# Kernel optimization log

Measured on AMD Instinct MI355X. Metric: run time of the kernel, lower is better.

The kernel has to match this reference:

```python
import jax, jax.numpy as jnp
import numpy as np

N_NODES = 100000
N_EDGES = 600000
D = 128
L = 4
BN_EPS = 1e-5


def setup_inputs() -> dict:
    key = jax.random.key(0)
    ks = jax.random.split(key, 12)
    x = jax.random.normal(ks[0], (N_NODES, D), dtype=jnp.float32)
    edge_index = jax.random.randint(ks[1], (2, N_EDGES), 0, N_NODES, dtype=jnp.int64)
    edge_attr = jax.random.uniform(ks[2], (N_EDGES, 1), dtype=jnp.float32)
    s = 0.05
    return {
        'x': x,
        'edge_index': edge_index,
        'edge_attr': edge_attr,
        'We': jax.random.normal(ks[3], (L, 1, D), dtype=jnp.float32) * s,   # GINE edge projection Linear(1, D)
        'be': jnp.zeros((L, D), dtype=jnp.float32),
        'eps': jnp.zeros((L,), dtype=jnp.float32),                          # train_eps=True, init 0
        'W1': jax.random.normal(ks[4], (L, D, D), dtype=jnp.float32) * s,
        'b1': jnp.zeros((L, D), dtype=jnp.float32),
        'gamma': jnp.ones((L, D), dtype=jnp.float32),
        'beta': jnp.zeros((L, D), dtype=jnp.float32),
        'W2': jax.random.normal(ks[5], (L, D, D), dtype=jnp.float32) * s,
        'b2': jnp.zeros((L, D), dtype=jnp.float32),
    }


def _gine_layer(h, src, dst, edge_attr, We, be, eps, W1, b1, gamma, beta, W2, b2):
    n = h.shape[0]
    e = edge_attr @ We + be                       # [E, D] edge embedding
    m = jax.nn.relu(h[src] + e)                   # gather + add + relu (messages)
    agg = jax.ops.segment_sum(m, dst, num_segments=n)  # scatter-add to destination nodes
    z = (1.0 + eps) * h + agg
    # MLP: Linear -> BatchNorm1d (training stats) -> ReLU -> Linear
    z = z @ W1 + b1
    mu = jnp.mean(z, axis=0)
    var = jnp.var(z, axis=0)                      # biased var, as in torch BN training
    z = (z - mu) * jax.lax.rsqrt(var + BN_EPS) * gamma + beta
    z = jax.nn.relu(z)
    return z @ W2 + b2


def reference(x, edge_index, edge_attr, We, be, eps, W1, b1, gamma, beta, W2, b2):
    src, dst = edge_index[0], edge_index[1]
    h = x
    for l in range(L):
        z = _gine_layer(h, src, dst, edge_attr, We[l], be[l], eps[l],
                        W1[l], b1[l], gamma[l], beta[l], W2[l], b2[l])
        r = jax.nn.relu(z)
        h = r if l == 0 else h + r
    return h
```

## Files before the change

kernel.cpp:

```cpp
#include <hip/hip_runtime.h>

#define NN 100000
#define NE 600000
#define DD 128
#define NL 4
#define GB 512

typedef __attribute__((ext_vector_type(8))) short short8;
typedef __attribute__((ext_vector_type(4))) float float4v;

__device__ inline unsigned short f2bf(float f) {
  union { float f; unsigned u; } v; v.f = f;
  unsigned r = v.u + 0x7fff + ((v.u >> 16) & 1);
  return (unsigned short)(r >> 16);
}
__device__ inline float bf2f(unsigned short u) {
  union { unsigned u; float f; } v; v.u = ((unsigned)u) << 16;
  return v.f;
}

__global__ void k_h2b(const float* __restrict__ src, unsigned short* __restrict__ dst,
                      float* __restrict__ stats4, int* __restrict__ counts) {
  int i = blockIdx.x * 256 + threadIdx.x;
  if (i < NL * 256) stats4[i] = 0.f;
  if (i < NN) counts[i] = 0;
  if (i >= NN * DD / 4) return;
  float4 v = ((const float4*)src)[i];
  ushort4 o;
  o.x = f2bf(v.x); o.y = f2bf(v.y); o.z = f2bf(v.z); o.w = f2bf(v.w);
  ((ushort4*)dst)[i] = o;
}

__global__ void k_prep(const float* __restrict__ W1, const float* __restrict__ W2,
                       unsigned short* __restrict__ WT) {
  int i = blockIdx.x * 256 + threadIdx.x;
  if (i >= 8 * 16384) return;
  int m = i >> 14;
  int el = i & 16383;
  int k = el >> 7;
  int n = el & 127;
  const float* src = (m < 4) ? (W1 + (size_t)m * 16384) : (W2 + (size_t)(m - 4) * 16384);
  WT[(size_t)m * 16384 + n * 128 + k] = f2bf(src[k * 128 + n]);
}

__global__ void k_count(const int* __restrict__ ei, int* __restrict__ counts) {
  int e = blockIdx.x * 256 + threadIdx.x;
  if (e < NE) atomicAdd(&counts[ei[NE + e]], 1);
}

#define ST 256
#define SC 2
#define SB ((NN + ST * SC - 1) / (ST * SC))

__global__ void k_scan_part(const int* __restrict__ counts, int* __restrict__ row_ptr,
                            int* __restrict__ bsums) {
  __shared__ int s[ST];
  int b = blockIdx.x, t = threadIdx.x;
  int base = b * (ST * SC) + t * SC;
  int v0 = (base < NN) ? counts[base] : 0;
  int v1 = (base + 1 < NN) ? counts[base + 1] : 0;
  int tsum = v0 + v1;
  s[t] = tsum;
  __syncthreads();
  for (int d = 1; d < ST; d <<= 1) {
    int x = (t >= d) ? s[t - d] : 0;
    __syncthreads();
    s[t] += x;
    __syncthreads();
  }
  int excl = s[t] - tsum;
  if (base < NN) row_ptr[base] = excl;
  if (base + 1 < NN) row_ptr[base + 1] = excl + v0;
  if (t == ST - 1) bsums[b] = s[t];
}

__global__ void k_scan_bsum(const int* __restrict__ bsums, int* __restrict__ boffs,
                            int* __restrict__ row_ptr) {
  __shared__ int s[ST];
  int t = threadIdx.x;
  int v = (t < SB) ? bsums[t] : 0;
  s[t] = v;
  __syncthreads();
  for (int d = 1; d < ST; d <<= 1) {
    int x = (t >= d) ? s[t - d] : 0;
    __syncthreads();
    s[t] += x;
    __syncthreads();
  }
  if (t < SB) boffs[t] = s[t] - v;
  if (t == ST - 1) row_ptr[NN] = s[t];
}

__global__ void k_scan_add(const int* __restrict__ boffs, int* __restrict__ row_ptr,
                           int* __restrict__ off) {
  int b = blockIdx.x, t = threadIdx.x;
  int base = b * (ST * SC) + t * SC;
  int o = boffs[b];
  if (base < NN) { row_ptr[base] += o; off[base] = 0; }
  if (base + 1 < NN) { row_ptr[base + 1] += o; off[base + 1] = 0; }
}

__global__ void k_fill(const int* __restrict__ ei, const float* __restrict__ attr,
                       const int* __restrict__ row_ptr, int* __restrict__ off,
                       int2* __restrict__ csr) {
  int e = blockIdx.x * 256 + threadIdx.x;
  if (e >= NE) return;
  int srcv = ei[e];
  int dstv = ei[NE + e];
  int pos = atomicAdd(&off[dstv], 1);
  int idx = row_ptr[dstv] + pos;
  csr[idx] = make_int2(srcv, __float_as_int(attr[e]));
}

__global__ void k_agg(const unsigned short* __restrict__ hb,
                      const int* __restrict__ row_ptr, const int2* __restrict__ csr,
                      const float* __restrict__ We, const float* __restrict__ be,
                      const float* __restrict__ epsp, unsigned short* __restrict__ zb) {
  int gid = blockIdx.x * blockDim.x + threadIdx.x;
  int n = gid >> 6;
  int lane = gid & 63;
  if (n >= NN) return;
  int d0 = lane * 2;
  float we0 = We[d0], we1 = We[d0 + 1];
  float be0 = be[d0], be1 = be[d0 + 1];
  int b = row_ptr[n], e = row_ptr[n + 1];
  int deg = e - b;
  int cnt = (deg < 64) ? deg : 64;
  int2 rec = (lane < cnt) ? csr[b + lane] : make_int2(0, 0);
  int myidx = rec.x;
  float myatt = __int_as_float(rec.y);
  if (lane >= cnt) myatt = 0.f;
  float acc0 = 0.f, acc1 = 0.f;
  int i = 0;
  for (; i + 4 <= cnt; i += 4) {
    int s0 = __shfl(myidx, i);
    int s1 = __shfl(myidx, i + 1);
    int s2 = __shfl(myidx, i + 2);
    int s3 = __shfl(myidx, i + 3);
    float a0 = __shfl(myatt, i);
    float a1 = __shfl(myatt, i + 1);
    float a2 = __shfl(myatt, i + 2);
    float a3 = __shfl(myatt, i + 3);
    unsigned hv0 = *(const unsigned*)(hb + (size_t)s0 * DD + d0);
    unsigned hv1 = *(const unsigned*)(hb + (size_t)s1 * DD + d0);
    unsigned hv2 = *(const unsigned*)(hb + (size_t)s2 * DD + d0);
    unsigned hv3 = *(const unsigned*)(hb + (size_t)s3 * DD + d0);
    acc0 += fmaxf(bf2f((unsigned short)(hv0 & 0xffffu)) + fmaf(a0, we0, be0), 0.f);
    acc1 += fmaxf(bf2f((unsigned short)(hv0 >> 16)) + fmaf(a0, we1, be1), 0.f);
    acc0 += fmaxf(bf2f((unsigned short)(hv1 & 0xffffu)) + fmaf(a1, we0, be0), 0.f);
    acc1 += fmaxf(bf2f((unsigned short)(hv1 >> 16)) + fmaf(a1, we1, be1), 0.f);
    acc0 += fmaxf(bf2f((unsigned short)(hv2 & 0xffffu)) + fmaf(a2, we0, be0), 0.f);
    acc1 += fmaxf(bf2f((unsigned short)(hv2 >> 16)) + fmaf(a2, we1, be1), 0.f);
    acc0 += fmaxf(bf2f((unsigned short)(hv3 & 0xffffu)) + fmaf(a3, we0, be0), 0.f);
    acc1 += fmaxf(bf2f((unsigned short)(hv3 >> 16)) + fmaf(a3, we1, be1), 0.f);
  }
  for (; i < cnt; i++) {
    int s = __shfl(myidx, i);
    float a = __shfl(myatt, i);
    unsigned hv = *(const unsigned*)(hb + (size_t)s * DD + d0);
    acc0 += fmaxf(bf2f((unsigned short)(hv & 0xffffu)) + fmaf(a, we0, be0), 0.f);
    acc1 += fmaxf(bf2f((unsigned short)(hv >> 16)) + fmaf(a, we1, be1), 0.f);
  }
  for (int j = b + 64; j < e; j++) {
    int2 r2 = csr[j];
    float a = __int_as_float(r2.y);
    unsigned hv = *(const unsigned*)(hb + (size_t)r2.x * DD + d0);
    acc0 += fmaxf(bf2f((unsigned short)(hv & 0xffffu)) + fmaf(a, we0, be0), 0.f);
    acc1 += fmaxf(bf2f((unsigned short)(hv >> 16)) + fmaf(a, we1, be1), 0.f);
  }
  float ep = 1.f + epsp[0];
  unsigned hs = *(const unsigned*)(hb + (size_t)n * DD + d0);
  float zx = fmaf(ep, bf2f((unsigned short)(hs & 0xffffu)), acc0);
  float zy = fmaf(ep, bf2f((unsigned short)(hs >> 16)), acc1);
  unsigned pk = (unsigned)f2bf(zx) | ((unsigned)f2bf(zy) << 16);
  *(unsigned*)(zb + (size_t)n * DD + d0) = pk;
}

template <int MODE>
__global__ __launch_bounds__(256, 2) void k_gemm(
    const unsigned short* __restrict__ Xb, const unsigned short* __restrict__ WT,
    const float* __restrict__ bias, float* __restrict__ stats,
    const float* __restrict__ gamma, const float* __restrict__ beta,
    const float* __restrict__ hprev, float* __restrict__ Yout,
    unsigned short* __restrict__ Ybf) {
  __shared__ unsigned short Wl[128 * 136];
  __shared__ unsigned short Xl[2][64 * 136];
  __shared__ float bns[256];
  const int tid = threadIdx.x;
  const int G = gridDim.x;
  const int NT = (NN + 63) >> 6;

  for (int i = tid; i < 2048; i += 256) {
    int rr = i >> 4, c = i & 15;
    *(uint4*)&Wl[rr * 136 + c * 8] = *(const uint4*)&WT[rr * 128 + c * 8];
  }

  const int lane = tid & 63;
  const int w = tid >> 6;
  const int m = lane & 15;
  const int quad = lane >> 4;

  const int c8 = tid & 15, rr16 = tid >> 4;
  float scl[8], sfl[8];
  if (MODE >= 1) {
    if (tid < 128) {
      const float invN = 1.f / (float)NN;
      float mu = stats[tid] * invN;
      float var = fmaxf(stats[128 + tid] * invN - mu * mu, 0.f);
      float xx = var + 1e-5f;
      float r = rsqrtf(xx);
      r = r * (1.5f - 0.5f * xx * r * r);
      float scale = gamma[tid] * r;
      bns[tid] = scale;
      bns[128 + tid] = beta[tid] - mu * scale;
    }
    __syncthreads();
#pragma unroll
    for (int j = 0; j < 8; j++) {
      scl[j] = bns[c8 * 8 + j];
      sfl[j] = bns[128 + c8 * 8 + j];
    }
  }

  uint4 xu[4];
  auto LOADR = [&](int t) {
    int r0 = t << 6;
#pragma unroll
    for (int it = 0; it < 4; it++) {
      int gr = r0 + rr16 + it * 16;
      xu[it] = (gr < NN) ? *(const uint4*)(Xb + (size_t)gr * DD + c8 * 8)
                         : make_uint4(0u, 0u, 0u, 0u);
    }
  };
  auto STORE_LDS = [&](int b) {
#pragma unroll
    for (int it = 0; it < 4; it++) {
      int row = rr16 + it * 16;
      uint4 u = xu[it];
      if (MODE >= 1) {
        unsigned p[4] = {u.x, u.y, u.z, u.w};
#pragma unroll
        for (int j = 0; j < 4; j++) {
          float lo = bf2f((unsigned short)(p[j] & 0xffffu));
          float hi = bf2f((unsigned short)(p[j] >> 16));
          lo = fmaxf(fmaf(lo, scl[2 * j], sfl[2 * j]), 0.f);
          hi = fmaxf(fmaf(hi, scl[2 * j + 1], sfl[2 * j + 1]), 0.f);
          p[j] = (unsigned)f2bf(lo) | ((unsigned)f2bf(hi) << 16);
        }
        u = make_uint4(p[0], p[1], p[2], p[3]);
      }
      *(uint4*)&Xl[b][row * 136 + c8 * 8] = u;
    }
  };

  float4v ssum[8], ssq[8];
  if (MODE == 0) {
#pragma unroll
    for (int ct = 0; ct < 8; ct++) {
      ssum[ct] = (float4v){0.f, 0.f, 0.f, 0.f};
      ssq[ct] = (float4v){0.f, 0.f, 0.f, 0.f};
    }
  }

  const int t0 = blockIdx.x;
  LOADR(t0);
  STORE_LDS(0);
  if (t0 + G < NT) LOADR(t0 + G);
  __syncthreads();

  int buf = 0;
  for (int t = t0; t < NT; t += G) {
    const int nxt = t + G;
    if (nxt < NT) {
      STORE_LDS(buf ^ 1);
      if (nxt + G < NT) LOADR(nxt + G);
    }

    float4v acc[8];
#pragma unroll
    for (int ct = 0; ct < 8; ct++) {
      float4 b4 = *(const float4*)&bias[ct * 16 + quad * 4];
      acc[ct] = (float4v){b4.x, b4.y, b4.z, b4.w};
    }

    const unsigned short* Ap = &Wl[m * 136 + quad * 8];
    const unsigned short* Bp = &Xl[buf][(w * 16 + m) * 136 + quad * 8];
#pragma unroll
    for (int q = 0; q < 4; q++) {
      short8 bfrag = *(const short8*)(Bp + q * 32);
#pragma unroll
      for (int ct = 0; ct < 8; ct++) {
        short8 afrag = *(const short8*)(Ap + ct * 16 * 136 + q * 32);
        acc[ct] = __builtin_amdgcn_mfma_f32_16x16x32_bf16(afrag, bfrag, acc[ct], 0, 0, 0);
      }
    }

    asm volatile("s_waitcnt lgkmcnt(0)" ::: "memory");
    __builtin_amdgcn_s_barrier();

    const int r = (t << 6) + w * 16 + m;
    if (r < NN) {
      const size_t rb = (size_t)r * DD;
#pragma unroll
      for (int ct = 0; ct < 8; ct++) {
        float4v v = acc[ct];
        const int col = ct * 16 + quad * 4;
        if (MODE == 0) {
          ssum[ct] += v;
          ssq[ct] += v * v;
          ushort4 o;
          o.x = f2bf(v[0]); o.y = f2bf(v[1]); o.z = f2bf(v[2]); o.w = f2bf(v[3]);
          *(ushort4*)&Ybf[rb + col] = o;
        } else {
          v[0] = fmaxf(v[0], 0.f); v[1] = fmaxf(v[1], 0.f);
          v[2] = fmaxf(v[2], 0.f); v[3] = fmaxf(v[3], 0.f);
          if (MODE == 2) {
            float4 hp = *(const float4*)&hprev[rb + col];
            v[0] += hp.x; v[1] += hp.y; v[2] += hp.z; v[3] += hp.w;
          }
          *(float4v*)&Yout[rb + col] = v;
          if (Ybf) {
            ushort4 o;
            o.x = f2bf(v[0]); o.y = f2bf(v[1]); o.z = f2bf(v[2]); o.w = f2bf(v[3]);
            *(ushort4*)&Ybf[rb + col] = o;
          }
        }
      }
    }
    buf ^= 1;
  }

  if (MODE == 0) {
    float* sarr = (float*)Xl;
    float* sqarr = sarr + 512;
#pragma unroll
    for (int ct = 0; ct < 8; ct++) {
      float4v s = ssum[ct], s2 = ssq[ct];
#pragma unroll
      for (int d = 1; d < 16; d <<= 1) {
#pragma unroll
        for (int j = 0; j < 4; j++) {
          s[j] += __shfl_xor(s[j], d);
          s2[j] += __shfl_xor(s2[j], d);
        }
      }
      if (m == 0) {
        *(float4v*)&sarr[w * 128 + ct * 16 + quad * 4] = s;
        *(float4v*)&sqarr[w * 128 + ct * 16 + quad * 4] = s2;
      }
    }
    __syncthreads();
    if (tid < 128) {
      atomicAdd(&stats[tid], sarr[tid] + sarr[128 + tid] + sarr[256 + tid] + sarr[384 + tid]);
    } else {
      int c = tid - 128;
      atomicAdd(&stats[128 + c], sqarr[c] + sqarr[128 + c] + sqarr[256 + c] + sqarr[384 + c]);
    }
  }
}

static inline size_t align256(size_t x) { return (x + 255) & ~(size_t)255; }

extern "C" void kernel_launch(void* const* d_in, const int* in_sizes, int n_in,
                              void* d_out, int out_size, void* d_ws, size_t ws_size,
                              hipStream_t stream) {
  const float* x     = (const float*)d_in[0];
  const int*   ei    = (const int*)d_in[1];
  const float* attr  = (const float*)d_in[2];
  const float* We    = (const float*)d_in[3];
  const float* be    = (const float*)d_in[4];
  const float* eps   = (const float*)d_in[5];
  const float* W1    = (const float*)d_in[6];
  const float* b1    = (const float*)d_in[7];
  const float* gamma = (const float*)d_in[8];
  const float* beta  = (const float*)d_in[9];
  const float* W2    = (const float*)d_in[10];
  const float* b2    = (const float*)d_in[11];
  float* out = (float*)d_out;

  char* w = (char*)d_ws;
  unsigned short* z2 = (unsigned short*)w; w += align256((size_t)NN * DD * 2);
  unsigned short* hb = (unsigned short*)w; w += align256((size_t)NN * DD * 2);
  unsigned short* zb = (unsigned short*)w; w += align256((size_t)NN * DD * 2);
  int*   row_ptr  = (int*)w;   w += align256((size_t)(NN + 1) * 4);
  int*   counts   = (int*)w;   w += align256((size_t)NN * 4);
  int*   off      = (int*)w;   w += align256((size_t)NN * 4);
  int2*  csr      = (int2*)w;  w += align256((size_t)NE * 8);
  float* stats4   = (float*)w; w += align256((size_t)NL * 256 * 4);
  int*   bsums    = (int*)w;   w += align256(ST * 4);
  int*   boffs    = (int*)w;   w += align256(ST * 4);
  unsigned short* WTb = (unsigned short*)w; w += align256((size_t)8 * 16384 * 2);

  k_prep<<<512, 256, 0, stream>>>(W1, W2, WTb);
  k_h2b<<<(NN * DD / 4 + 255) / 256, 256, 0, stream>>>(x, hb, stats4, counts);
  k_count<<<(NE + 255) / 256, 256, 0, stream>>>(ei, counts);
  k_scan_part<<<SB, ST, 0, stream>>>(counts, row_ptr, bsums);
  k_scan_bsum<<<1, ST, 0, stream>>>(bsums, boffs, row_ptr);
  k_scan_add<<<SB, ST, 0, stream>>>(boffs, row_ptr, off);
  k_fill<<<(NE + 255) / 256, 256, 0, stream>>>(ei, attr, row_ptr, off, csr);

  for (int l = 0; l < NL; l++) {
    float* st = stats4 + (size_t)l * 256;
    k_agg<<<(NN * 64 + 255) / 256, 256, 0, stream>>>(
        hb, row_ptr, csr, We + l * DD, be + l * DD, eps + l, zb);
    k_gemm<0><<<GB, 256, 0, stream>>>(zb, WTb + (size_t)l * 16384, b1 + l * DD,
                                      st, nullptr, nullptr, nullptr, nullptr, z2);
    unsigned short* hbo = (l < NL - 1) ? hb : nullptr;
    if (l == 0)
      k_gemm<1><<<GB, 256, 0, stream>>>(z2, WTb + (size_t)(4 + l) * 16384, b2 + l * DD,
                                        st, gamma + l * DD, beta + l * DD,
                                        nullptr, out, hbo);
    else
      k_gemm<2><<<GB, 256, 0, stream>>>(z2, WTb + (size_t)(4 + l) * 16384, b2 + l * DD,
                                        st, gamma + l * DD, beta + l * DD,
                                        out, out, hbo);
  }
}
```

Measured before the change: 573.1 us.

## Use 16 lanes per node with 16-byte gathers in aggregation; fuse prep kernels

The aggregation kernel now assigns 16 lanes per node, each loading 8 bf16 features with a single 16-byte load, instead of 64 lanes loading 4 bytes each. This cuts wavefront count and issues wider gather loads. The in-wave edge prefetch window shrinks from 64 to 16, so nodes with higher degree fall back to the serial tail loop. Separately, counter and stats zeroing move into the weight-prep kernel and edge counting is fused into the bf16 conversion kernel, removing one launch.

Measured after the change: 532.8 us. 1.08x faster.

```diff
diff --git a/kernel.cpp b/kernel.cpp
--- a/kernel.cpp
+++ b/kernel.cpp
@@ -19,21 +19,12 @@
   return v.f;
 }
 
-__global__ void k_h2b(const float* __restrict__ src, unsigned short* __restrict__ dst,
-                      float* __restrict__ stats4, int* __restrict__ counts) {
+__global__ void k_prep(const float* __restrict__ W1, const float* __restrict__ W2,
+                       unsigned short* __restrict__ WT, int* __restrict__ counts,
+                       float* __restrict__ stats4) {
   int i = blockIdx.x * 256 + threadIdx.x;
+  if (i < NN) counts[i] = 0;
   if (i < NL * 256) stats4[i] = 0.f;
-  if (i < NN) counts[i] = 0;
-  if (i >= NN * DD / 4) return;
-  float4 v = ((const float4*)src)[i];
-  ushort4 o;
-  o.x = f2bf(v.x); o.y = f2bf(v.y); o.z = f2bf(v.z); o.w = f2bf(v.w);
-  ((ushort4*)dst)[i] = o;
-}
-
-__global__ void k_prep(const float* __restrict__ W1, const float* __restrict__ W2,
-                       unsigned short* __restrict__ WT) {
-  int i = blockIdx.x * 256 + threadIdx.x;
   if (i >= 8 * 16384) return;
   int m = i >> 14;
   int el = i & 16383;
@@ -43,9 +34,15 @@
   WT[(size_t)m * 16384 + n * 128 + k] = f2bf(src[k * 128 + n]);
 }
 
-__global__ void k_count(const int* __restrict__ ei, int* __restrict__ counts) {
-  int e = blockIdx.x * 256 + threadIdx.x;
-  if (e < NE) atomicAdd(&counts[ei[NE + e]], 1);
+__global__ void k_h2b(const float* __restrict__ src, unsigned short* __restrict__ dst,
+                      const int* __restrict__ ei, int* __restrict__ counts) {
+  int i = blockIdx.x * 256 + threadIdx.x;
+  if (i < NE) atomicAdd(&counts[ei[NE + i]], 1);
+  if (i >= NN * DD / 4) return;
+  float4 v = ((const float4*)src)[i];
+  ushort4 o;
+  o.x = f2bf(v.x); o.y = f2bf(v.y); o.z = f2bf(v.z); o.w = f2bf(v.w);
+  ((ushort4*)dst)[i] = o;
 }
 
 #define ST 256
@@ -112,68 +109,89 @@
   csr[idx] = make_int2(srcv, __float_as_int(attr[e]));
 }
 
+#define CONSUME(hv, a)                                                                   \
+  do {                                                                                   \
+    acc0.x += fmaxf(__uint_as_float((hv).x << 16)          + fmaf((a), we0.x, be0.x), 0.f); \
+    acc0.y += fmaxf(__uint_as_float((hv).x & 0xffff0000u)  + fmaf((a), we0.y, be0.y), 0.f); \
+    acc0.z += fmaxf(__uint_as_float((hv).y << 16)          + fmaf((a), we0.z, be0.z), 0.f); \
+    acc0.w += fmaxf(__uint_as_float((hv).y & 0xffff0000u)  + fmaf((a), we0.w, be0.w), 0.f); \
+    acc1.x += fmaxf(__uint_as_float((hv).z << 16)          + fmaf((a), we1.x, be1.x), 0.f); \
+    acc1.y += fmaxf(__uint_as_float((hv).z & 0xffff0000u)  + fmaf((a), we1.y, be1.y), 0.f); \
+    acc1.z += fmaxf(__uint_as_float((hv).w << 16)          + fmaf((a), we1.z, be1.z), 0.f); \
+    acc1.w += fmaxf(__uint_as_float((hv).w & 0xffff0000u)  + fmaf((a), we1.w, be1.w), 0.f); \
+  } while (0)
+
 __global__ void k_agg(const unsigned short* __restrict__ hb,
                       const int* __restrict__ row_ptr, const int2* __restrict__ csr,
                       const float* __restrict__ We, const float* __restrict__ be,
                       const float* __restrict__ epsp, unsigned short* __restrict__ zb) {
   int gid = blockIdx.x * blockDim.x + threadIdx.x;
-  int n = gid >> 6;
-  int lane = gid & 63;
+  int n = gid >> 4;
+  int li = gid & 15;
   if (n >= NN) return;
-  int d0 = lane * 2;
-  float we0 = We[d0], we1 = We[d0 + 1];
-  float be0 = be[d0], be1 = be[d0 + 1];
+  int d0 = li * 8;
+  float4 we0 = *(const float4*)(We + d0);
+  float4 we1 = *(const float4*)(We + d0 + 4);
+  float4 be0 = *(const float4*)(be + d0);
+  float4 be1 = *(const float4*)(be + d0 + 4);
   int b = row_ptr[n], e = row_ptr[n + 1];
   int deg = e - b;
-  int cnt = (deg < 64) ? deg : 64;
-  int2 rec = (lane < cnt) ? csr[b + lane] : make_int2(0, 0);
+  int cnt = (deg < 16) ? deg : 16;
+  int2 rec = (li < cnt) ? csr[b + li] : make_int2(0, 0);
   int myidx = rec.x;
   float myatt = __int_as_float(rec.y);
-  if (lane >= cnt) myatt = 0.f;
-  float acc0 = 0.f, acc1 = 0.f;
+
+  float4 acc0 = make_float4(0.f, 0.f, 0.f, 0.f);
+  float4 acc1 = make_float4(0.f, 0.f, 0.f, 0.f);
+
   int i = 0;
   for (; i + 4 <= cnt; i += 4) {
-    int s0 = __shfl(myidx, i);
-    int s1 = __shfl(myidx, i + 1);
-    int s2 = __shfl(myidx, i + 2);
-    int s3 = __shfl(myidx, i + 3);
-    float a0 = __shfl(myatt, i);
-    float a1 = __shfl(myatt, i + 1);
-    float a2 = __shfl(myatt, i + 2);
-    float a3 = __shfl(myatt, i + 3);
-    unsigned hv0 = *(const unsigned*)(hb + (size_t)s0 * DD + d0);
-    unsigned hv1 = *(const unsigned*)(hb + (size_t)s1 * DD + d0);
-    unsigned hv2 = *(const unsigned*)(hb + (size_t)s2 * DD + d0);
-    unsigned hv3 = *(const unsigned*)(hb + (size_t)s3 * DD + d0);
-    acc0 += fmaxf(bf2f((unsigned short)(hv0 & 0xffffu)) + fmaf(a0, we0, be0), 0.f);
-    acc1 += fmaxf(bf2f((unsigned short)(hv0 >> 16)) + fmaf(a0, we1, be1), 0.f);
-    acc0 += fmaxf(bf2f((unsigned short)(hv1 & 0xffffu)) + fmaf(a1, we0, be0), 0.f);
-    acc1 += fmaxf(bf2f((unsigned short)(hv1 >> 16)) + fmaf(a1, we1, be1), 0.f);
-    acc0 += fmaxf(bf2f((unsigned short)(hv2 & 0xffffu)) + fmaf(a2, we0, be0), 0.f);
-    acc1 += fmaxf(bf2f((unsigned short)(hv2 >> 16)) + fmaf(a2, we1, be1), 0.f);
-    acc0 += fmaxf(bf2f((unsigned short)(hv3 & 0xffffu)) + fmaf(a3, we0, be0), 0.f);
-    acc1 += fmaxf(bf2f((unsigned short)(hv3 >> 16)) + fmaf(a3, we1, be1), 0.f);
+    int s0 = __shfl(myidx, i, 16);
+    int s1 = __shfl(myidx, i + 1, 16);
+    int s2 = __shfl(myidx, i + 2, 16);
+    int s3 = __shfl(myidx, i + 3, 16);
+    float a0 = __shfl(myatt, i, 16);
+    float a1 = __shfl(myatt, i + 1, 16);
+    float a2 = __shfl(myatt, i + 2, 16);
+    float a3 = __shfl(myatt, i + 3, 16);
+    uint4 hv0 = *(const uint4*)(hb + (size_t)s0 * DD + d0);
+    uint4 hv1 = *(const uint4*)(hb + (size_t)s1 * DD + d0);
+    uint4 hv2 = *(const uint4*)(hb + (size_t)s2 * DD + d0);
+    uint4 hv3 = *(const uint4*)(hb + (size_t)s3 * DD + d0);
+    CONSUME(hv0, a0);
+    CONSUME(hv1, a1);
+    CONSUME(hv2, a2);
+    CONSUME(hv3, a3);
   }
   for (; i < cnt; i++) {
-    int s = __shfl(myidx, i);
-    float a = __shfl(myatt, i);
-    unsigned hv = *(const unsigned*)(hb + (size_t)s * DD + d0);
-    acc0 += fmaxf(bf2f((unsigned short)(hv & 0xffffu)) + fmaf(a, we0, be0), 0.f);
-    acc1 += fmaxf(bf2f((unsigned short)(hv >> 16)) + fmaf(a, we1, be1), 0.f);
-  }
-  for (int j = b + 64; j < e; j++) {
+    int s = __shfl(myidx, i, 16);
+    float a = __shfl(myatt, i, 16);
+    uint4 hv = *(const uint4*)(hb + (size_t)s * DD + d0);
+    CONSUME(hv, a);
+  }
+  for (int j = b + 16; j < e; j++) {
     int2 r2 = csr[j];
     float a = __int_as_float(r2.y);
-    unsigned hv = *(const unsigned*)(hb + (size_t)r2.x * DD + d0);
-    acc0 += fmaxf(bf2f((unsigned short)(hv & 0xffffu)) + fmaf(a, we0, be0), 0.f);
-    acc1 += fmaxf(bf2f((unsigned short)(hv >> 16)) + fmaf(a, we1, be1), 0.f);
-  }
+    uint4 hv = *(const uint4*)(hb + (size_t)r2.x * DD + d0);
+    CONSUME(hv, a);
+  }
+
   float ep = 1.f + epsp[0];
-  unsigned hs = *(const unsigned*)(hb + (size_t)n * DD + d0);
-  float zx = fmaf(ep, bf2f((unsigned short)(hs & 0xffffu)), acc0);
-  float zy = fmaf(ep, bf2f((unsigned short)(hs >> 16)), acc1);
-  unsigned pk = (unsigned)f2bf(zx) | ((unsigned)f2bf(zy) << 16);
-  *(unsigned*)(zb + (size_t)n * DD + d0) = pk;
+  uint4 hs = *(const uint4*)(hb + (size_t)n * DD + d0);
+  float z0 = fmaf(ep, __uint_as_float(hs.x << 16), acc0.x);
+  float z1 = fmaf(ep, __uint_as_float(hs.x & 0xffff0000u), acc0.y);
+  float z2 = fmaf(ep, __uint_as_float(hs.y << 16), acc0.z);
+  float z3 = fmaf(ep, __uint_as_float(hs.y & 0xffff0000u), acc0.w);
+  float z4 = fmaf(ep, __uint_as_float(hs.z << 16), acc1.x);
+  float z5 = fmaf(ep, __uint_as_float(hs.z & 0xffff0000u), acc1.y);
+  float z6 = fmaf(ep, __uint_as_float(hs.w << 16), acc1.z);
+  float z7 = fmaf(ep, __uint_as_float(hs.w & 0xffff0000u), acc1.w);
+  uint4 o;
+  o.x = (unsigned)f2bf(z0) | ((unsigned)f2bf(z1) << 16);
+  o.y = (unsigned)f2bf(z2) | ((unsigned)f2bf(z3) << 16);
+  o.z = (unsigned)f2bf(z4) | ((unsigned)f2bf(z5) << 16);
+  o.w = (unsigned)f2bf(z6) | ((unsigned)f2bf(z7) << 16);
+  *(uint4*)(zb + (size_t)n * DD + d0) = o;
 }
 
 template <int MODE>
@@ -391,9 +409,8 @@
   int*   boffs    = (int*)w;   w += align256(ST * 4);
   unsigned short* WTb = (unsigned short*)w; w += align256((size_t)8 * 16384 * 2);
 
-  k_prep<<<512, 256, 0, stream>>>(W1, W2, WTb);
-  k_h2b<<<(NN * DD / 4 + 255) / 256, 256, 0, stream>>>(x, hb, stats4, counts);
-  k_count<<<(NE + 255) / 256, 256, 0, stream>>>(ei, counts);
+  k_prep<<<512, 256, 0, stream>>>(W1, W2, WTb, counts, stats4);
+  k_h2b<<<(NN * DD / 4 + 255) / 256, 256, 0, stream>>>(x, hb, ei, counts);
   k_scan_part<<<SB, ST, 0, stream>>>(counts, row_ptr, bsums);
   k_scan_bsum<<<1, ST, 0, stream>>>(bsums, boffs, row_ptr);
   k_scan_add<<<SB, ST, 0, stream>>>(boffs, row_ptr, off);
@@ -401,7 +418,7 @@
 
   for (int l = 0; l < NL; l++) {
     float* st = stats4 + (size_t)l * 256;
-    k_agg<<<(NN * 64 + 255) / 256, 256, 0, stream>>>(
+    k_agg<<<(NN * 16 + 255) / 256, 256, 0, stream>>>(
         hb, row_ptr, csr, We + l * DD, be + l * DD, eps + l, zb);
     k_gemm<0><<<GB, 256, 0, stream>>>(zb, WTb + (size_t)l * 16384, b1 + l * DD,
                                       st, nullptr, nullptr, nullptr, nullptr, z2);
```
